# Kernel optimization log

Measured on AMD Instinct MI355X. Metric: run time of the kernel, lower is better.

## Reference

```python
import jax, jax.numpy as jnp
import numpy as np

HEAD_DIM = 64
HIDDEN_SIZE = 3072
NUM_HEADS = 48
B, TXT, VID = 1, 256, 1792
N = TXT + VID


def _layernorm(x, g, b, eps=1e-5):
    mu = jnp.mean(x, axis=-1, keepdims=True)
    xc = x - mu
    var = jnp.mean(xc * xc, axis=-1, keepdims=True)
    return xc * jax.lax.rsqrt(var + eps) * g + b


def _apply_rope1(x, freqs):
    # x: [B, L, H, D]; freqs: [1, 1, Lf, D//2, 2, 2]
    Bx, L, H, D = x.shape
    x_ = x.reshape(Bx, L, H, D // 2, 1, 2)
    # faithful to torch: if dim-2 sizes mismatch (H vs Lf), slice freqs to H
    if x_.shape[2] != 1 and freqs.shape[2] != 1 and x_.shape[2] != freqs.shape[2]:
        freqs = freqs[:, :, : x_.shape[2]]
    out = freqs[..., 0] * x_[..., 0] + freqs[..., 1] * x_[..., 1]
    return out.reshape(Bx, L, H, D).astype(x.dtype)


def setup_inputs() -> dict:
    key = jax.random.key(0)
    ks = jax.random.split(key, 16)
    s = 1.0 / np.sqrt(HIDDEN_SIZE)
    d = dict(
        combined=jax.random.normal(ks[0], (B, N, HIDDEN_SIZE), jnp.float32),
        freqs=jax.random.normal(ks[1], (1, 1, VID, HEAD_DIM // 2, 2, 2), jnp.float32),
        Wq=jax.random.normal(ks[2], (HIDDEN_SIZE, HIDDEN_SIZE), jnp.float32) * s,
        bq=jnp.zeros((HIDDEN_SIZE,), jnp.float32),
        Wk=jax.random.normal(ks[3], (HIDDEN_SIZE, HIDDEN_SIZE), jnp.float32) * s,
        bk=jnp.zeros((HIDDEN_SIZE,), jnp.float32),
        Wv=jax.random.normal(ks[4], (HIDDEN_SIZE, HIDDEN_SIZE), jnp.float32) * s,
        bv=jnp.zeros((HIDDEN_SIZE,), jnp.float32),
        Wo=jax.random.normal(ks[5], (HIDDEN_SIZE, HIDDEN_SIZE), jnp.float32) * s,
        bo=jnp.zeros((HIDDEN_SIZE,), jnp.float32),
        gq=jnp.ones((HEAD_DIM,), jnp.float32),
        bgq=jnp.zeros((HEAD_DIM,), jnp.float32),
        gk=jnp.ones((HEAD_DIM,), jnp.float32),
        bgk=jnp.zeros((HEAD_DIM,), jnp.float32),
        txt_len=TXT,
    )
    return d


def reference(combined, freqs, Wq, bq, Wk, bk, Wv, bv, Wo, bo, gq, bgq, gk, bgk, txt_len):
    Bx, Nx, _ = combined.shape
    Q = (combined @ Wq.T + bq).reshape(Bx, Nx, NUM_HEADS, HEAD_DIM)
    K = (combined @ Wk.T + bk).reshape(Bx, Nx, NUM_HEADS, HEAD_DIM)
    V = (combined @ Wv.T + bv).reshape(Bx, Nx, NUM_HEADS, HEAD_DIM)
    Q = _layernorm(Q, gq, bgq)
    K = _layernorm(K, gk, bgk)
    if freqs is not None and Nx - txt_len > 0:
        Q_vid = _apply_rope1(Q[:, txt_len:], freqs)
        K_vid = _apply_rope1(K[:, txt_len:], freqs)
        Q = jnp.concatenate([Q[:, :txt_len], Q_vid], axis=1)
        K = jnp.concatenate([K[:, :txt_len], K_vid], axis=1)
    # SDPA in fp32: [B, H, N, D]
    q = Q.transpose(0, 2, 1, 3).astype(jnp.float32)
    k = K.transpose(0, 2, 1, 3).astype(jnp.float32)
    v = V.transpose(0, 2, 1, 3).astype(jnp.float32)
    scale = 1.0 / np.sqrt(HEAD_DIM)
    scores = jnp.einsum('bhqd,bhkd->bhqk', q, k) * scale
    probs = jax.nn.softmax(scores, axis=-1)
    attn = jnp.einsum('bhqk,bhkd->bhqd', probs, v).astype(combined.dtype)
    attn = attn.transpose(0, 2, 1, 3).reshape(Bx, Nx, HIDDEN_SIZE)
    out = attn @ Wo.T + bo
    return out[:, txt_len:], out[:, :txt_len]
```

## Files before the change

kernel.cpp:

```cpp
#include <hip/hip_runtime.h>
#include <hip/hip_bf16.h>

typedef __attribute__((ext_vector_type(8))) short bf16x8;
typedef __attribute__((ext_vector_type(4))) float f32x4;
typedef unsigned int __attribute__((address_space(1))) as1_uint;
typedef unsigned int __attribute__((address_space(3))) as3_uint;

#define TXT 256
#define VIDN 1792
#define SEQ 2048
#define HID 3072
#define NH 48
#define HD 64
#define QSCALE 0.18033688011112042f

__device__ __forceinline__ unsigned short f2bf(float f) {
  union { float f; unsigned int u; } x; x.f = f;
  unsigned int r = x.u + 0x7fffu + ((x.u >> 16) & 1u);
  return (unsigned short)(r >> 16);
}

__device__ __forceinline__ void gload16(const void* g, void* l) {
  __builtin_amdgcn_global_load_lds((const as1_uint*)g, (as3_uint*)l, 16, 0, 0);
}

__device__ __forceinline__ void fbar() {
  asm volatile("" ::: "memory");
  __builtin_amdgcn_s_barrier();
  asm volatile("" ::: "memory");
}

__global__ __launch_bounds__(256) void cvt_kernel(const float* __restrict__ s,
                                                  unsigned short* __restrict__ d, int n) {
  int i = (blockIdx.x * 256 + threadIdx.x) * 4;
  if (i >= n) return;
  float4 v = *(const float4*)(s + i);
  ushort4 o;
  o.x = f2bf(v.x); o.y = f2bf(v.y); o.z = f2bf(v.z); o.w = f2bf(v.w);
  *(ushort4*)(d + i) = o;
}

__global__ __launch_bounds__(256) void cvt4_kernel(
    const float* __restrict__ comb, const float* __restrict__ wq,
    const float* __restrict__ wk, const float* __restrict__ wv,
    unsigned short* __restrict__ abf, unsigned short* __restrict__ wqkv) {
  const int CB = (SEQ * HID) / 1024;
  const int WB = (HID * HID) / 1024;
  int bid = blockIdx.x;
  const float* s; unsigned short* d; int r;
  if (bid < CB) { s = comb; d = abf; r = bid; }
  else {
    int q = bid - CB; int m = q / WB; r = q - m * WB;
    s = (m == 0) ? wq : (m == 1) ? wk : wv;
    d = wqkv + (size_t)m * HID * HID;
  }
  int i = (r * 256 + threadIdx.x) * 4;
  float4 v = *(const float4*)(s + i);
  ushort4 o;
  o.x = f2bf(v.x); o.y = f2bf(v.y); o.z = f2bf(v.z); o.w = f2bf(v.w);
  *(ushort4*)(d + i) = o;
}

template<int MODE>
__global__ __launch_bounds__(512, 4) void gemm256(
    const unsigned short* __restrict__ A,
    const unsigned short* __restrict__ Bt,
    int K, int ntn,
    float* __restrict__ Cq, unsigned short* __restrict__ Vt, const float* __restrict__ bv,
    float* __restrict__ Cout, const float* __restrict__ bo)
{
  __shared__ unsigned short lds[3 * 8192];
  const int tid = threadIdx.x;
  const int mt = blockIdx.x / ntn, nt = blockIdx.x % ntn;
  const int m0 = mt * 128, n0 = nt * 128;
  const int w = tid >> 6, lane = tid & 63, lr = lane & 15, lg = lane >> 4;
  const int wr = w >> 2, wc = w & 3;
  f32x4 acc[4][2] = {};
  const int NT = K >> 5;

  const int soff  = tid * 16;
  const int soffs = soff ^ (((soff >> 7) & 3) << 4);
  const int srow  = soffs >> 6;
  const int scol  = (soffs & 63) >> 1;
  const unsigned short* Asrc = A + (size_t)(m0 + srow) * K + scol;
  const unsigned short* Bsrc = Bt + (size_t)(n0 + srow) * K + scol;

  int aoff[4], boff[2];
#pragma unroll
  for (int mf = 0; mf < 4; ++mf) {
    int arow = wr * 64 + mf * 16 + lr;
    aoff[mf] = arow * 32 + (lg ^ ((arow >> 1) & 3)) * 8;
  }
#pragma unroll
  for (int nf = 0; nf < 2; ++nf) {
    int brow = wc * 32 + nf * 16 + lr;
    boff[nf] = brow * 32 + (lg ^ ((brow >> 1) & 3)) * 8;
  }

#define STAGE(t)                                                               \
  {                                                                            \
    const int slot_ = (t) % 3;                                                 \
    const int k0_ = (t) << 5;                                                  \
    char* base_ = (char*)lds + slot_ * 16384;                                  \
    gload16(Asrc + k0_, base_ + soff);                                         \
    gload16(Bsrc + k0_, base_ + 8192 + soff);                                  \
  }

#define COMPUTE(t)                                                             \
  {                                                                            \
    const unsigned short* lA = lds + ((t) % 3) * 8192;                         \
    const unsigned short* lB = lA + 4096;                                      \
    bf16x8 bfr[2];                                                             \
    _Pragma("unroll")                                                          \
    for (int nf = 0; nf < 2; ++nf)                                             \
      bfr[nf] = *(const bf16x8*)&lB[boff[nf]];                                 \
    __builtin_amdgcn_s_setprio(1);                                             \
    _Pragma("unroll")                                                          \
    for (int mf = 0; mf < 4; ++mf) {                                           \
      bf16x8 af = *(const bf16x8*)&lA[aoff[mf]];                               \
      acc[mf][0] = __builtin_amdgcn_mfma_f32_16x16x32_bf16(af, bfr[0], acc[mf][0], 0, 0, 0); \
      acc[mf][1] = __builtin_amdgcn_mfma_f32_16x16x32_bf16(af, bfr[1], acc[mf][1], 0, 0, 0); \
    }                                                                          \
    __builtin_amdgcn_s_setprio(0);                                             \
  }

  STAGE(0); STAGE(1);
  int t = 0;
  for (; t < NT - 2; ++t) {
    STAGE(t + 2);
    asm volatile("s_waitcnt vmcnt(4)" ::: "memory");
    fbar();
    COMPUTE(t);
    fbar();
  }
  asm volatile("s_waitcnt vmcnt(2)" ::: "memory");
  fbar();
  COMPUTE(t); ++t;
  fbar();
  asm volatile("s_waitcnt vmcnt(0)" ::: "memory");
  fbar();
  COMPUTE(t);
#undef STAGE
#undef COMPUTE

  if (MODE == 0) {
    if (n0 < 6144) {
#pragma unroll
      for (int mf = 0; mf < 4; ++mf) {
        int row = m0 + wr * 64 + mf * 16 + lg * 4;
#pragma unroll
        for (int nf = 0; nf < 2; ++nf) {
          int col = n0 + wc * 32 + nf * 16 + lr;
#pragma unroll
          for (int j = 0; j < 4; ++j)
            Cq[(size_t)(row + j) * 6144 + col] = acc[mf][nf][j];
        }
      }
    } else {
#pragma unroll
      for (int mf = 0; mf < 4; ++mf) {
        int srow2 = m0 + wr * 64 + mf * 16 + lg * 4;
#pragma unroll
        for (int nf = 0; nf < 2; ++nf) {
          int n2 = n0 - 6144 + wc * 32 + nf * 16 + lr;
          float b = bv[n2];
          ushort4 pk;
          pk.x = f2bf(acc[mf][nf][0] + b);
          pk.y = f2bf(acc[mf][nf][1] + b);
          pk.z = f2bf(acc[mf][nf][2] + b);
          pk.w = f2bf(acc[mf][nf][3] + b);
          *(ushort4*)(Vt + (size_t)n2 * SEQ + srow2) = pk;
        }
      }
    }
  } else {
#pragma unroll
    for (int mf = 0; mf < 4; ++mf) {
      int row = m0 + wr * 64 + mf * 16 + lg * 4;
#pragma unroll
      for (int nf = 0; nf < 2; ++nf) {
        int col = n0 + wc * 32 + nf * 16 + lr;
        float b = bo[col];
#pragma unroll
        for (int j = 0; j < 4; ++j) {
          int s = row + j;
          int orow = (s >= TXT) ? (s - TXT) : (VIDN + s);
          Cout[(size_t)orow * HID + col] = acc[mf][nf][j] + b;
        }
      }
    }
  }
}

__global__ __launch_bounds__(256) void ln_rope_kernel(
    const float* __restrict__ QK,
    const float* __restrict__ bq, const float* __restrict__ bk,
    const float* __restrict__ gq, const float* __restrict__ bgq,
    const float* __restrict__ gk, const float* __restrict__ bgk,
    const float* __restrict__ freqs,
    unsigned short* __restrict__ Qh, unsigned short* __restrict__ Kh)
{
  int wid = blockIdx.x * 4 + (threadIdx.x >> 6);
  int lane = threadIdx.x & 63;
  int s = wid / 96;
  int rem = wid - s * 96;
  int h = rem >> 1, qk = rem & 1;
  int col = h * 64 + lane;
  float x = QK[(size_t)s * 6144 + qk * 3072 + col] + (qk ? bk[col] : bq[col]);
  float m = x;
#pragma unroll
  for (int msk = 1; msk < 64; msk <<= 1) m += __shfl_xor(m, msk);
  float mu = m * (1.0f / 64.0f);
  float xc = x - mu;
  float v = xc * xc;
#pragma unroll
  for (int msk = 1; msk < 64; msk <<= 1) v += __shfl_xor(v, msk);
  float rstd = rsqrtf(v * (1.0f / 64.0f) + 1e-5f);
  float y = xc * rstd * (qk ? gk[lane] : gq[lane]) + (qk ? bgk[lane] : bgq[lane]);
  if (s >= TXT) {
    float p = __shfl_xor(y, 1);
    float xe = (lane & 1) ? p : y;
    float xo = (lane & 1) ? y : p;
    int base = h * 128 + (lane >> 1) * 4 + (lane & 1) * 2;
    y = freqs[base] * xe + freqs[base + 1] * xo;
  }
  if (!qk) y *= QSCALE;
  (qk ? Kh : Qh)[((size_t)h * SEQ + s) * 64 + lane] = f2bf(y);
}

__global__ __launch_bounds__(512) void fattn_kernel(
    const unsigned short* __restrict__ Qh, const unsigned short* __restrict__ Kh,
    const unsigned short* __restrict__ Vt, unsigned short* __restrict__ ctx)
{
  __shared__ unsigned short kt[2][2][64][32];
  __shared__ unsigned short vt[2][2][64][32];
  __shared__ unsigned short pl[8][16][72];
  const int h = blockIdx.x >> 4;
  const int q0 = (blockIdx.x & 15) * 128;
  const int tid = threadIdx.x, w = tid >> 6, lane = tid & 63, lr = lane & 15, lg = lane >> 4;

  bf16x8 qf0, qf1;
  {
    const unsigned short* qp = Qh + ((size_t)h * SEQ + q0 + w * 16 + lr) * 64 + lg * 8;
    qf0 = *(const bf16x8*)qp;
    qf1 = *(const bf16x8*)(qp + 32);
  }
  f32x4 oacc[4] = {};
  float mrun = -1e30f, lrun = 0.f;

  const int soff = tid * 16;
  const int shalf = soff >> 12;
  const int srem = soff & 4095;
  const int srow = srem >> 6, scb = srem & 63;
  const unsigned short* Ksrc = Kh + ((size_t)h * SEQ + srow) * 64 + shalf * 32 + (scb >> 1);
  const unsigned short* Vsrc = Vt + ((size_t)(h * 64 + srow)) * SEQ + shalf * 32 + (scb >> 1);

#define FSTAGE(t)                                                              \
  {                                                                            \
    const int sl_ = (t) & 1;                                                   \
    const int kv0_ = (t) << 6;                                                 \
    gload16(Ksrc + (size_t)kv0_ * 64, (char*)kt + sl_ * 8192 + soff);          \
    gload16(Vsrc + kv0_, (char*)vt + sl_ * 8192 + soff);                       \
  }

  FSTAGE(0);
  for (int t = 0; t < 32; ++t) {
    const int sl = t & 1;
    if (t < 31) {
      FSTAGE(t + 1);
      asm volatile("s_waitcnt vmcnt(2)" ::: "memory");
    } else {
      asm volatile("s_waitcnt vmcnt(0)" ::: "memory");
    }
    fbar();

    f32x4 sacc[4] = {};
    __builtin_amdgcn_s_setprio(1);
#pragma unroll
    for (int nf = 0; nf < 4; ++nf) {
      bf16x8 a0 = *(const bf16x8*)&kt[sl][0][nf * 16 + lr][lg * 8];
      bf16x8 a1 = *(const bf16x8*)&kt[sl][1][nf * 16 + lr][lg * 8];
      sacc[nf] = __builtin_amdgcn_mfma_f32_16x16x32_bf16(a0, qf0, sacc[nf], 0, 0, 0);
      sacc[nf] = __builtin_amdgcn_mfma_f32_16x16x32_bf16(a1, qf1, sacc[nf], 0, 0, 0);
    }
    __builtin_amdgcn_s_setprio(0);

    float mx;
    {
      float t0 = fmaxf(fmaxf(sacc[0][0], sacc[0][1]), fmaxf(sacc[0][2], sacc[0][3]));
      float t1 = fmaxf(fmaxf(sacc[1][0], sacc[1][1]), fmaxf(sacc[1][2], sacc[1][3]));
      float t2 = fmaxf(fmaxf(sacc[2][0], sacc[2][1]), fmaxf(sacc[2][2], sacc[2][3]));
      float t3 = fmaxf(fmaxf(sacc[3][0], sacc[3][1]), fmaxf(sacc[3][2], sacc[3][3]));
      mx = fmaxf(fmaxf(t0, t1), fmaxf(t2, t3));
    }
    mx = fmaxf(mx, __shfl_xor(mx, 16));
    mx = fmaxf(mx, __shfl_xor(mx, 32));

    if (!__all(mx <= mrun + 8.0f)) {
      float mn = fmaxf(mrun, mx);
      float corr = exp2f(mrun - mn);
      lrun *= corr;
      mrun = mn;
      float c0 = __shfl(corr, lg * 4 + 0);
      float c1 = __shfl(corr, lg * 4 + 1);
      float c2 = __shfl(corr, lg * 4 + 2);
      float c3 = __shfl(corr, lg * 4 + 3);
#pragma unroll
      for (int df = 0; df < 4; ++df) {
        oacc[df][0] *= c0; oacc[df][1] *= c1;
        oacc[df][2] *= c2; oacc[df][3] *= c3;
      }
    }

    float pr[4][4];
#pragma unroll
    for (int nf = 0; nf < 4; ++nf)
#pragma unroll
      for (int r = 0; r < 4; ++r)
        pr[nf][r] = exp2f(sacc[nf][r] - mrun);
    float rs;
    {
      float s0 = (pr[0][0] + pr[0][1]) + (pr[0][2] + pr[0][3]);
      float s1 = (pr[1][0] + pr[1][1]) + (pr[1][2] + pr[1][3]);
      float s2 = (pr[2][0] + pr[2][1]) + (pr[2][2] + pr[2][3]);
      float s3 = (pr[3][0] + pr[3][1]) + (pr[3][2] + pr[3][3]);
      rs = (s0 + s1) + (s2 + s3);
    }
    rs += __shfl_xor(rs, 16);
    rs += __shfl_xor(rs, 32);
    lrun += rs;

#pragma unroll
    for (int nf = 0; nf < 4; ++nf) {
      union { __hip_bfloat162 h; unsigned int u; } c0, c1;
      c0.h = __float22bfloat162_rn(make_float2(pr[nf][0], pr[nf][1]));
      c1.h = __float22bfloat162_rn(make_float2(pr[nf][2], pr[nf][3]));
      uint2 pw; pw.x = c0.u; pw.y = c1.u;
      *(uint2*)&pl[w][lr][nf * 16 + lg * 4] = pw;
    }

    bf16x8 pa0 = *(const bf16x8*)&pl[w][lr][lg * 8];
    bf16x8 pa1 = *(const bf16x8*)&pl[w][lr][32 + lg * 8];
    __builtin_amdgcn_s_setprio(1);
#pragma unroll
    for (int df = 0; df < 4; ++df) {
      bf16x8 v0 = *(const bf16x8*)&vt[sl][0][df * 16 + lr][lg * 8];
      bf16x8 v1 = *(const bf16x8*)&vt[sl][1][df * 16 + lr][lg * 8];
      oacc[df] = __builtin_amdgcn_mfma_f32_16x16x32_bf16(pa0, v0, oacc[df], 0, 0, 0);
      oacc[df] = __builtin_amdgcn_mfma_f32_16x16x32_bf16(pa1, v1, oacc[df], 0, 0, 0);
    }
    __builtin_amdgcn_s_setprio(0);

    fbar();
  }
#undef FSTAGE

  float linv = 1.0f / lrun;
  float i0 = __shfl(linv, lg * 4 + 0);
  float i1 = __shfl(linv, lg * 4 + 1);
  float i2 = __shfl(linv, lg * 4 + 2);
  float i3 = __shfl(linv, lg * 4 + 3);
#pragma unroll
  for (int df = 0; df < 4; ++df) {
    int s = q0 + w * 16 + lg * 4;
    int dcol = h * 64 + df * 16 + lr;
    ctx[(size_t)(s + 0) * HID + dcol] = f2bf(oacc[df][0] * i0);
    ctx[(size_t)(s + 1) * HID + dcol] = f2bf(oacc[df][1] * i1);
    ctx[(size_t)(s + 2) * HID + dcol] = f2bf(oacc[df][2] * i2);
    ctx[(size_t)(s + 3) * HID + dcol] = f2bf(oacc[df][3] * i3);
  }
}

extern "C" void kernel_launch(void* const* d_in, const int* in_sizes, int n_in,
                              void* d_out, int out_size, void* d_ws, size_t ws_size,
                              hipStream_t stream) {
  const float* combined = (const float*)d_in[0];
  const float* freqs    = (const float*)d_in[1];
  const float* Wq  = (const float*)d_in[2];
  const float* bq  = (const float*)d_in[3];
  const float* Wk  = (const float*)d_in[4];
  const float* bk  = (const float*)d_in[5];
  const float* Wv  = (const float*)d_in[6];
  const float* bv  = (const float*)d_in[7];
  const float* Wo  = (const float*)d_in[8];
  const float* bo  = (const float*)d_in[9];
  const float* gq  = (const float*)d_in[10];
  const float* bgq = (const float*)d_in[11];
  const float* gk  = (const float*)d_in[12];
  const float* bgk = (const float*)d_in[13];
  float* out = (float*)d_out;

  char* ws = (char*)d_ws;
  unsigned short* Abf  = (unsigned short*)ws; ws += (size_t)SEQ * HID * 2;
  unsigned short* Wqkv = (unsigned short*)ws; ws += (size_t)3 * HID * HID * 2;
  float*          QK   = (float*)ws;          ws += (size_t)SEQ * 6144 * 4;
  unsigned short* Qh   = (unsigned short*)ws; ws += (size_t)NH * SEQ * HD * 2;
  unsigned short* Kh   = (unsigned short*)ws; ws += (size_t)NH * SEQ * HD * 2;
  unsigned short* Vt   = (unsigned short*)ws; ws += (size_t)NH * HD * SEQ * 2;
  unsigned short* Wob  = (unsigned short*)QK;
  unsigned short* ctx  = Abf;

  cvt4_kernel<<<(SEQ * HID) / 1024 + 3 * (HID * HID) / 1024, 256, 0, stream>>>(
      combined, Wq, Wk, Wv, Abf, Wqkv);

  gemm256<0><<<16 * 72, 512, 0, stream>>>(Abf, Wqkv, HID, 72, QK, Vt, bv, nullptr, nullptr);

  ln_rope_kernel<<<(SEQ * NH * 2) / 4, 256, 0, stream>>>(QK, bq, bk, gq, bgq, gk, bgk, freqs, Qh, Kh);

  cvt_kernel<<<(HID * HID) / 1024, 256, 0, stream>>>(Wo, Wob, HID * HID);

  fattn_kernel<<<NH * 16, 512, 0, stream>>>(Qh, Kh, Vt, ctx);

  gemm256<1><<<16 * 24, 512, 0, stream>>>(ctx, Wob, HID, 24, nullptr, nullptr, nullptr, out, bo);
}
```

Before: 405.7 us.

## Enlarge GEMM tiles to 128x256 with BK=64 and interleaved load/MFMA pipeline

Replaces the 128x128, BK=32 GEMM with a 128x256 tile and BK=64 K-step. Global-to-LDS loads for the next stage are split into four chunks, each issued between MFMA groups. The wider tile doubles operand reuse per LDS read and halves the number of blocks, cutting global traffic and barrier count per FLOP. In exchange it uses 144KB of LDS per block and more accumulator registers, so occupancy drops. The output GEMM also gets only 192 blocks, which may underfill the GPU.

```diff
diff --git a/kernel.cpp b/kernel.cpp
--- a/kernel.cpp
+++ b/kernel.cpp
@@ -62,86 +62,136 @@
 }
 
 template<int MODE>
-__global__ __launch_bounds__(512, 4) void gemm256(
+__global__ __launch_bounds__(512) void gemm8p(
     const unsigned short* __restrict__ A,
     const unsigned short* __restrict__ Bt,
     int K, int ntn,
     float* __restrict__ Cq, unsigned short* __restrict__ Vt, const float* __restrict__ bv,
     float* __restrict__ Cout, const float* __restrict__ bo)
 {
-  __shared__ unsigned short lds[3 * 8192];
+  __shared__ unsigned short lds[3 * 24576];
   const int tid = threadIdx.x;
   const int mt = blockIdx.x / ntn, nt = blockIdx.x % ntn;
-  const int m0 = mt * 128, n0 = nt * 128;
+  const int m0 = mt * 128, n0 = nt * 256;
   const int w = tid >> 6, lane = tid & 63, lr = lane & 15, lg = lane >> 4;
   const int wr = w >> 2, wc = w & 3;
-  f32x4 acc[4][2] = {};
-  const int NT = K >> 5;
-
-  const int soff  = tid * 16;
-  const int soffs = soff ^ (((soff >> 7) & 3) << 4);
-  const int srow  = soffs >> 6;
-  const int scol  = (soffs & 63) >> 1;
-  const unsigned short* Asrc = A + (size_t)(m0 + srow) * K + scol;
-  const unsigned short* Bsrc = Bt + (size_t)(n0 + srow) * K + scol;
-
-  int aoff[4], boff[2];
-#pragma unroll
-  for (int mf = 0; mf < 4; ++mf) {
-    int arow = wr * 64 + mf * 16 + lr;
-    aoff[mf] = arow * 32 + (lg ^ ((arow >> 1) & 3)) * 8;
-  }
-#pragma unroll
-  for (int nf = 0; nf < 2; ++nf) {
-    int brow = wc * 32 + nf * 16 + lr;
-    boff[nf] = brow * 32 + (lg ^ ((brow >> 1) & 3)) * 8;
-  }
-
-#define STAGE(t)                                                               \
+  f32x4 acc[4][4] = {};
+  const int NT = K >> 6;
+
+  const unsigned short *As0, *As1, *Bs0, *Bs1, *Bs2, *Bs3;
+  int ao0, ao1, bb0, bb1, bb2, bb3;
+  {
+    int so, ss;
+    so = tid * 16;          ss = so ^ (((so >> 7) & 7) << 4);
+    ao0 = so; As0 = A + (size_t)(m0 + (ss >> 7)) * K + ((ss & 127) >> 1);
+    so = (512 + tid) * 16;  ss = so ^ (((so >> 7) & 7) << 4);
+    ao1 = so; As1 = A + (size_t)(m0 + (ss >> 7)) * K + ((ss & 127) >> 1);
+    so = tid * 16;          ss = so ^ (((so >> 7) & 7) << 4);
+    bb0 = so; Bs0 = Bt + (size_t)(n0 + (ss >> 7)) * K + ((ss & 127) >> 1);
+    so = (512 + tid) * 16;  ss = so ^ (((so >> 7) & 7) << 4);
+    bb1 = so; Bs1 = Bt + (size_t)(n0 + (ss >> 7)) * K + ((ss & 127) >> 1);
+    so = (1024 + tid) * 16; ss = so ^ (((so >> 7) & 7) << 4);
+    bb2 = so; Bs2 = Bt + (size_t)(n0 + (ss >> 7)) * K + ((ss & 127) >> 1);
+    so = (1536 + tid) * 16; ss = so ^ (((so >> 7) & 7) << 4);
+    bb3 = so; Bs3 = Bt + (size_t)(n0 + (ss >> 7)) * K + ((ss & 127) >> 1);
+  }
+
+  int ra[2][4], rb[2][4];
+#pragma unroll
+  for (int h = 0; h < 2; ++h) {
+#pragma unroll
+    for (int f = 0; f < 4; ++f) {
+      int r1 = wr * 64 + f * 16 + lr;
+      ra[h][f] = (r1 * 64 + h * 32 + lg * 8) ^ ((r1 & 7) << 3);
+      int r2 = wc * 64 + f * 16 + lr;
+      rb[h][f] = (r2 * 64 + h * 32 + lg * 8) ^ ((r2 & 7) << 3);
+    }
+  }
+
+#define STAGE_ALL(t)                                                           \
   {                                                                            \
-    const int slot_ = (t) % 3;                                                 \
-    const int k0_ = (t) << 5;                                                  \
-    char* base_ = (char*)lds + slot_ * 16384;                                  \
-    gload16(Asrc + k0_, base_ + soff);                                         \
-    gload16(Bsrc + k0_, base_ + 8192 + soff);                                  \
-  }
-
-#define COMPUTE(t)                                                             \
+    char* sb_ = (char*)lds + ((t) % 3) * 49152;                                \
+    const int kk_ = (t) << 6;                                                  \
+    gload16(As0 + kk_, sb_ + ao0);                                             \
+    gload16(As1 + kk_, sb_ + ao1);                                             \
+    gload16(Bs0 + kk_, sb_ + 16384 + bb0);                                     \
+    gload16(Bs1 + kk_, sb_ + 16384 + bb1);                                     \
+    gload16(Bs2 + kk_, sb_ + 16384 + bb2);                                     \
+    gload16(Bs3 + kk_, sb_ + 16384 + bb3);                                     \
+  }
+
+#define MM8(N0, N1)                                                            \
+  __builtin_amdgcn_s_setprio(1);                                               \
+  acc[0][N0] = __builtin_amdgcn_mfma_f32_16x16x32_bf16(af0, bq0, acc[0][N0], 0, 0, 0); \
+  acc[1][N0] = __builtin_amdgcn_mfma_f32_16x16x32_bf16(af1, bq0, acc[1][N0], 0, 0, 0); \
+  acc[2][N0] = __builtin_amdgcn_mfma_f32_16x16x32_bf16(af2, bq0, acc[2][N0], 0, 0, 0); \
+  acc[3][N0] = __builtin_amdgcn_mfma_f32_16x16x32_bf16(af3, bq0, acc[3][N0], 0, 0, 0); \
+  acc[0][N1] = __builtin_amdgcn_mfma_f32_16x16x32_bf16(af0, bq1, acc[0][N1], 0, 0, 0); \
+  acc[1][N1] = __builtin_amdgcn_mfma_f32_16x16x32_bf16(af1, bq1, acc[1][N1], 0, 0, 0); \
+  acc[2][N1] = __builtin_amdgcn_mfma_f32_16x16x32_bf16(af2, bq1, acc[2][N1], 0, 0, 0); \
+  acc[3][N1] = __builtin_amdgcn_mfma_f32_16x16x32_bf16(af3, bq1, acc[3][N1], 0, 0, 0); \
+  __builtin_amdgcn_s_setprio(0);
+
+#define ITER(t, SG, VMC)                                                       \
   {                                                                            \
-    const unsigned short* lA = lds + ((t) % 3) * 8192;                         \
-    const unsigned short* lB = lA + 4096;                                      \
-    bf16x8 bfr[2];                                                             \
-    _Pragma("unroll")                                                          \
-    for (int nf = 0; nf < 2; ++nf)                                             \
-      bfr[nf] = *(const bf16x8*)&lB[boff[nf]];                                 \
-    __builtin_amdgcn_s_setprio(1);                                             \
-    _Pragma("unroll")                                                          \
-    for (int mf = 0; mf < 4; ++mf) {                                           \
-      bf16x8 af = *(const bf16x8*)&lA[aoff[mf]];                               \
-      acc[mf][0] = __builtin_amdgcn_mfma_f32_16x16x32_bf16(af, bfr[0], acc[mf][0], 0, 0, 0); \
-      acc[mf][1] = __builtin_amdgcn_mfma_f32_16x16x32_bf16(af, bfr[1], acc[mf][1], 0, 0, 0); \
-    }                                                                          \
-    __builtin_amdgcn_s_setprio(0);                                             \
-  }
-
-  STAGE(0); STAGE(1);
+    const unsigned short* lA = lds + ((t) % 3) * 24576;                        \
+    const unsigned short* lB = lA + 8192;                                      \
+    char* sb = (char*)lds + (((t) + 2) % 3) * 49152;                           \
+    const int kk = ((t) + 2) << 6;                                             \
+    bf16x8 af0, af1, af2, af3, bq0, bq1;                                       \
+                                                \
+    af0 = *(const bf16x8*)&lA[ra[0][0]];                                       \
+    af1 = *(const bf16x8*)&lA[ra[0][1]];                                       \
+    af2 = *(const bf16x8*)&lA[ra[0][2]];                                       \
+    af3 = *(const bf16x8*)&lA[ra[0][3]];                                       \
+    bq0 = *(const bf16x8*)&lB[rb[0][0]];                                       \
+    bq1 = *(const bf16x8*)&lB[rb[0][1]];                                       \
+    if (SG) { gload16(As0 + kk, sb + ao0); gload16(As1 + kk, sb + ao1); }      \
+    fbar();                                                                    \
+    MM8(0, 1)                                                                  \
+    fbar();                                                                    \
+                                                \
+    bq0 = *(const bf16x8*)&lB[rb[0][2]];                                       \
+    bq1 = *(const bf16x8*)&lB[rb[0][3]];                                       \
+    if (SG) { gload16(Bs0 + kk, sb + 16384 + bb0);                             \
+              gload16(Bs1 + kk, sb + 16384 + bb1); }                           \
+    fbar();                                                                    \
+    MM8(2, 3)                                                                  \
+    fbar();                                                                    \
+                                                \
+    af0 = *(const bf16x8*)&lA[ra[1][0]];                                       \
+    af1 = *(const bf16x8*)&lA[ra[1][1]];                                       \
+    af2 = *(const bf16x8*)&lA[ra[1][2]];                                       \
+    af3 = *(const bf16x8*)&lA[ra[1][3]];                                       \
+    bq0 = *(const bf16x8*)&lB[rb[1][0]];                                       \
+    bq1 = *(const bf16x8*)&lB[rb[1][1]];                                       \
+    if (SG) { gload16(Bs2 + kk, sb + 16384 + bb2);                             \
+              gload16(Bs3 + kk, sb + 16384 + bb3); }                           \
+    fbar();                                                                    \
+    MM8(0, 1)                                                                  \
+    fbar();                                                                    \
+                      \
+    bq0 = *(const bf16x8*)&lB[rb[1][2]];                                       \
+    bq1 = *(const bf16x8*)&lB[rb[1][3]];                                       \
+    VMC;                                                                       \
+    fbar();                                                                    \
+    MM8(2, 3)                                                                  \
+    fbar();                                                                    \
+  }
+
+  STAGE_ALL(0);
+  STAGE_ALL(1);
+  asm volatile("s_waitcnt vmcnt(6)" ::: "memory");
+  fbar();
   int t = 0;
-  for (; t < NT - 2; ++t) {
-    STAGE(t + 2);
-    asm volatile("s_waitcnt vmcnt(4)" ::: "memory");
-    fbar();
-    COMPUTE(t);
-    fbar();
-  }
-  asm volatile("s_waitcnt vmcnt(2)" ::: "memory");
-  fbar();
-  COMPUTE(t); ++t;
-  fbar();
-  asm volatile("s_waitcnt vmcnt(0)" ::: "memory");
-  fbar();
-  COMPUTE(t);
-#undef STAGE
-#undef COMPUTE
+  for (; t < NT - 2; ++t)
+    ITER(t, 1, asm volatile("s_waitcnt vmcnt(6)" ::: "memory"));
+  ITER(t, 0, asm volatile("s_waitcnt vmcnt(0)" ::: "memory"));
+  ++t;
+  ITER(t, 0, ((void)0));
+#undef STAGE_ALL
+#undef MM8
+#undef ITER
 
   if (MODE == 0) {
     if (n0 < 6144) {
@@ -149,8 +199,8 @@
       for (int mf = 0; mf < 4; ++mf) {
         int row = m0 + wr * 64 + mf * 16 + lg * 4;
 #pragma unroll
-        for (int nf = 0; nf < 2; ++nf) {
-          int col = n0 + wc * 32 + nf * 16 + lr;
+        for (int nf = 0; nf < 4; ++nf) {
+          int col = n0 + wc * 64 + nf * 16 + lr;
 #pragma unroll
           for (int j = 0; j < 4; ++j)
             Cq[(size_t)(row + j) * 6144 + col] = acc[mf][nf][j];
@@ -161,8 +211,8 @@
       for (int mf = 0; mf < 4; ++mf) {
         int srow2 = m0 + wr * 64 + mf * 16 + lg * 4;
 #pragma unroll
-        for (int nf = 0; nf < 2; ++nf) {
-          int n2 = n0 - 6144 + wc * 32 + nf * 16 + lr;
+        for (int nf = 0; nf < 4; ++nf) {
+          int n2 = n0 - 6144 + wc * 64 + nf * 16 + lr;
           float b = bv[n2];
           ushort4 pk;
           pk.x = f2bf(acc[mf][nf][0] + b);
@@ -178,8 +228,8 @@
     for (int mf = 0; mf < 4; ++mf) {
       int row = m0 + wr * 64 + mf * 16 + lg * 4;
 #pragma unroll
-      for (int nf = 0; nf < 2; ++nf) {
-        int col = n0 + wc * 32 + nf * 16 + lr;
+      for (int nf = 0; nf < 4; ++nf) {
+        int col = n0 + wc * 64 + nf * 16 + lr;
         float b = bo[col];
 #pragma unroll
         for (int j = 0; j < 4; ++j) {
@@ -403,7 +453,7 @@
   cvt4_kernel<<<(SEQ * HID) / 1024 + 3 * (HID * HID) / 1024, 256, 0, stream>>>(
       combined, Wq, Wk, Wv, Abf, Wqkv);
 
-  gemm256<0><<<16 * 72, 512, 0, stream>>>(Abf, Wqkv, HID, 72, QK, Vt, bv, nullptr, nullptr);
+  gemm8p<0><<<16 * 36, 512, 0, stream>>>(Abf, Wqkv, HID, 36, QK, Vt, bv, nullptr, nullptr);
 
   ln_rope_kernel<<<(SEQ * NH * 2) / 4, 256, 0, stream>>>(QK, bq, bk, gq, bgq, gk, bgk, freqs, Qh, Kh);
 
@@ -411,5 +461,5 @@
 
   fattn_kernel<<<NH * 16, 512, 0, stream>>>(Qh, Kh, Vt, ctx);
 
-  gemm256<1><<<16 * 24, 512, 0, stream>>>(ctx, Wob, HID, 24, nullptr, nullptr, nullptr, out, bo);
-}
+  gemm8p<1><<<16 * 12, 512, 0, stream>>>(ctx, Wob, HID, 12, nullptr, nullptr, nullptr, out, bo);
+}
```

Result: no change. 403.2 us (-0.6%).
